# Optimization experiments

Measured on AMD Instinct MI355X. Metric: run time of the kernel, lower is better.

The kernel has to match this reference:

```python
import jax, jax.numpy as jnp
import numpy as np

B, T, V = 8, 1024, 2048

def setup_inputs() -> dict:
    key = jax.random.key(0)
    k1, k2, k3 = jax.random.split(key, 3)
    idx = jax.random.randint(k1, (B, T), 0, V)
    v_weight = jnp.zeros((T, 1), dtype=jnp.float32) + 0.02 * jax.random.normal(k2, (T, 1), dtype=jnp.float32)
    W = 0.01 * jnp.ones((V, V), dtype=jnp.float32) + 0.001 * jax.random.normal(k3, (V, V), dtype=jnp.float32)
    return {"idx": idx, "v_weight": v_weight, "W": W}

def reference(idx, v_weight, W):
    Tn = idx.shape[1]
    Vn = W.shape[0]
    e = jax.nn.one_hot(idx, Vn, dtype=jnp.float32)            # [B,T,V]
    pos = jnp.arange(Tn)
    rel = jnp.maximum(pos[:, None] - pos[None, :], 0)          # [T,T] clamped relative positions
    causal = pos[:, None] >= pos[None, :]                      # True where attention allowed
    # Layer 1: positional attention (shared across batch)
    a1 = v_weight[rel, 0]                                      # [T,T] gather from v embedding
    a1 = jnp.where(causal, a1, -jnp.inf)
    a1 = jax.nn.softmax(a1, axis=-1)
    layer_one = jnp.einsum('ts,bsv->btv', a1, e)               # [B,T,V]
    key_t = layer_one @ W.T                                    # Linear without bias: x @ W^T
    # Layer 2: content attention
    a2 = jnp.einsum('btv,bsv->bts', e, key_t)                  # [B,T,T]
    a2 = jnp.where(causal[None], a2, -jnp.inf)
    a2 = jax.nn.softmax(a2, axis=-1)
    logits = jnp.einsum('bts,bsv->btv', a2, e)                 # [B,T,V]
    return logits
```

## Files before the change

### kernel.cpp

```cpp
#include <hip/hip_runtime.h>
#include <hip/hip_bf16.h>
#include <math.h>

#define Bn 8
#define Tn 1024
#define Vn 2048

typedef __attribute__((ext_vector_type(8))) __bf16 bf16x8;
typedef __attribute__((ext_vector_type(4))) float floatx4;

__global__ __launch_bounds__(1024) void k_prep(const float* __restrict__ vw,
                                               float* __restrict__ E,
                                               float* __restrict__ Cinv) {
    __shared__ float sc[Tn];
    int tid = threadIdx.x;
    float e = __expf(vw[tid]);
    E[tid] = e;
    sc[tid] = e;
    __syncthreads();
    for (int off = 1; off < Tn; off <<= 1) {
        float add = (tid >= off) ? sc[tid - off] : 0.0f;
        __syncthreads();
        sc[tid] += add;
        __syncthreads();
    }
    Cinv[tid] = 1.0f / sc[tid];
}

__global__ __launch_bounds__(256) void k_bt(const float* __restrict__ E,
                                            const float* __restrict__ Cinv,
                                            __hip_bfloat16* __restrict__ BT) {
    int s = blockIdx.x;
    int tid = threadIdx.x;
    float cinv = Cinv[s];
    int k0 = tid * 4;
    ushort u[4];
#pragma unroll
    for (int j = 0; j < 4; ++j) {
        int k = k0 + j;
        float v = (k <= s) ? E[s - k] * cinv : 0.0f;
        __hip_bfloat16 h = __float2bfloat16(v);
        u[j] = *reinterpret_cast<ushort*>(&h);
    }
    *reinterpret_cast<ushort4*>(&BT[(size_t)s * Tn + k0]) = make_ushort4(u[0], u[1], u[2], u[3]);
}

__global__ __launch_bounds__(256) void k_gather(const int* __restrict__ idx,
                                                const float* __restrict__ W,
                                                __hip_bfloat16* __restrict__ A) {
    int b = blockIdx.y, t = blockIdx.x, tid = threadIdx.x;
    int r = idx[b * Tn + t];
    const float* Wr = W + (size_t)r * Vn;
    int4 c4 = *reinterpret_cast<const int4*>(&idx[b * Tn + tid * 4]);
    ushort u[4];
    __hip_bfloat16 h;
    h = __float2bfloat16(Wr[c4.x]); u[0] = *reinterpret_cast<ushort*>(&h);
    h = __float2bfloat16(Wr[c4.y]); u[1] = *reinterpret_cast<ushort*>(&h);
    h = __float2bfloat16(Wr[c4.z]); u[2] = *reinterpret_cast<ushort*>(&h);
    h = __float2bfloat16(Wr[c4.w]); u[3] = *reinterpret_cast<ushort*>(&h);
    *reinterpret_cast<ushort4*>(&A[((size_t)(b * Tn + t)) * Tn + tid * 4]) =
        make_ushort4(u[0], u[1], u[2], u[3]);
}

#define TM 128
#define TN 128
#define BK 32
#define LDP 40

__global__ __launch_bounds__(256) void k_gemm(const __hip_bfloat16* __restrict__ A,
                                              const __hip_bfloat16* __restrict__ BT,
                                              float* __restrict__ Cout) {
    __shared__ __align__(16) __hip_bfloat16 As[TM][LDP];
    __shared__ __align__(16) __hip_bfloat16 Bs[TN][LDP];
    int b = blockIdx.z;
    int m0 = blockIdx.y * TM;
    int n0 = blockIdx.x * TN;
    int tid = threadIdx.x;
    int wave = tid >> 6, lane = tid & 63;
    int wm = (wave >> 1) * 64, wn = (wave & 1) * 64;
    int lrow = lane & 15, quad = lane >> 4;

    const __hip_bfloat16* Ab = A + (size_t)b * Tn * Tn;

    floatx4 acc[4][4];
#pragma unroll
    for (int i = 0; i < 4; ++i)
#pragma unroll
        for (int j = 0; j < 4; ++j) acc[i][j] = (floatx4){0.f, 0.f, 0.f, 0.f};

    for (int k0 = 0; k0 < Tn; k0 += BK) {
#pragma unroll
        for (int i = 0; i < 2; ++i) {
            int ch = tid + i * 256;
            int r = ch >> 2, c = (ch & 3) * 8;
            *reinterpret_cast<uint4*>(&As[r][c]) =
                *reinterpret_cast<const uint4*>(&Ab[(size_t)(m0 + r) * Tn + k0 + c]);
            *reinterpret_cast<uint4*>(&Bs[r][c]) =
                *reinterpret_cast<const uint4*>(&BT[(size_t)(n0 + r) * Tn + k0 + c]);
        }
        __syncthreads();
        bf16x8 af[4], bfr[4];
#pragma unroll
        for (int mi = 0; mi < 4; ++mi)
            af[mi] = *reinterpret_cast<const bf16x8*>(&As[wm + mi * 16 + lrow][quad * 8]);
#pragma unroll
        for (int ni = 0; ni < 4; ++ni)
            bfr[ni] = *reinterpret_cast<const bf16x8*>(&Bs[wn + ni * 16 + lrow][quad * 8]);
#pragma unroll
        for (int mi = 0; mi < 4; ++mi)
#pragma unroll
            for (int ni = 0; ni < 4; ++ni)
                acc[mi][ni] = __builtin_amdgcn_mfma_f32_16x16x32_bf16(af[mi], bfr[ni],
                                                                      acc[mi][ni], 0, 0, 0);
        __syncthreads();
    }

    float* Cb = Cout + (size_t)b * Tn * Tn;
#pragma unroll
    for (int mi = 0; mi < 4; ++mi)
#pragma unroll
        for (int ni = 0; ni < 4; ++ni)
#pragma unroll
            for (int r = 0; r < 4; ++r) {
                int row = m0 + wm + mi * 16 + quad * 4 + r;
                int col = n0 + wn + ni * 16 + lrow;
                Cb[(size_t)row * Tn + col] = acc[mi][ni][r];
            }
}

__global__ __launch_bounds__(256) void k_softscat(const float* __restrict__ a2raw,
                                                  const int* __restrict__ idx,
                                                  float* __restrict__ out) {
    __shared__ float sh[Vn];
    __shared__ float red[8];
    int t = blockIdx.x, b = blockIdx.y, tid = threadIdx.x;
    int wave = tid >> 6, lane = tid & 63;
#pragma unroll
    for (int i = 0; i < Vn / 256; ++i) sh[tid + i * 256] = 0.0f;

    const float* row = a2raw + ((size_t)b * Tn + t) * Tn;
    float4 v4 = *reinterpret_cast<const float4*>(&row[tid * 4]);
    int4 c4 = *reinterpret_cast<const int4*>(&idx[b * Tn + tid * 4]);
    int s0 = tid * 4;
    float v[4] = {v4.x, v4.y, v4.z, v4.w};
    float m = -INFINITY;
#pragma unroll
    for (int j = 0; j < 4; ++j) {
        if (s0 + j > t) v[j] = -INFINITY;
        m = fmaxf(m, v[j]);
    }
#pragma unroll
    for (int off = 32; off > 0; off >>= 1) m = fmaxf(m, __shfl_xor(m, off));
    if (lane == 0) red[wave] = m;
    __syncthreads();
    m = fmaxf(fmaxf(red[0], red[1]), fmaxf(red[2], red[3]));
    float e[4];
    float lsum = 0.f;
#pragma unroll
    for (int j = 0; j < 4; ++j) {
        e[j] = (s0 + j <= t) ? __expf(v[j] - m) : 0.0f;
        lsum += e[j];
    }
#pragma unroll
    for (int off = 32; off > 0; off >>= 1) lsum += __shfl_xor(lsum, off);
    if (lane == 0) red[4 + wave] = lsum;
    __syncthreads();
    float inv = 1.0f / (red[4] + red[5] + red[6] + red[7]);
    int c[4] = {c4.x, c4.y, c4.z, c4.w};
#pragma unroll
    for (int j = 0; j < 4; ++j)
        if (s0 + j <= t) atomicAdd(&sh[c[j]], e[j] * inv);
    __syncthreads();
    float* orow = out + ((size_t)b * Tn + t) * Vn;
#pragma unroll
    for (int i = 0; i < Vn / (256 * 4); ++i)
        *reinterpret_cast<float4*>(&orow[(tid + i * 256) * 4]) =
            *reinterpret_cast<const float4*>(&sh[(tid + i * 256) * 4]);
}

extern "C" void kernel_launch(void* const* d_in, const int* in_sizes, int n_in,
                              void* d_out, int out_size, void* d_ws, size_t ws_size,
                              hipStream_t stream) {
    const int* idx = (const int*)d_in[0];
    const float* vw = (const float*)d_in[1];
    const float* W = (const float*)d_in[2];
    float* out = (float*)d_out;
    char* ws = (char*)d_ws;

    float* E = (float*)(ws);
    float* Cinv = (float*)(ws + 4096);
    __hip_bfloat16* BT = (__hip_bfloat16*)(ws + 8192);
    __hip_bfloat16* Abf = (__hip_bfloat16*)(ws + 2105344);
    float* a2raw = (float*)(ws + 18882560);

    k_prep<<<1, 1024, 0, stream>>>(vw, E, Cinv);
    k_bt<<<dim3(Tn), 256, 0, stream>>>(E, Cinv, BT);
    k_gather<<<dim3(Tn, Bn), 256, 0, stream>>>(idx, W, Abf);
    k_gemm<<<dim3(Tn / TN, Tn / TM, Bn), 256, 0, stream>>>(Abf, BT, a2raw);
    k_softscat<<<dim3(Tn, Bn), 256, 0, stream>>>(a2raw, idx, out);
}
```

Measured before the change: 159.6 us.

## Exploit causal structure: skip masked GEMM tiles, fuse prep into k_bt

The GEMM grid now covers only the 36 lower-triangular 128x128 tiles per batch, and each tile's K loop stops at the diagonal, because BT is zero above it. This removes roughly half the tiles plus the wasted K work. The separate single-block prefix-sum prep kernel is dropped: each k_bt block recomputes its own normalizer with a block reduction over exp(vw), and the softmax kernel skips loading masked-out score chunks. Upper-triangle entries of a2raw are left unwritten, which is safe because they are always masked before use.

Result: faster. 149.7 us (-6.2%).

```diff
diff --git a/kernel.cpp b/kernel.cpp
--- a/kernel.cpp
+++ b/kernel.cpp
@@ -9,36 +9,30 @@
 typedef __attribute__((ext_vector_type(8))) __bf16 bf16x8;
 typedef __attribute__((ext_vector_type(4))) float floatx4;
 
-__global__ __launch_bounds__(1024) void k_prep(const float* __restrict__ vw,
-                                               float* __restrict__ E,
-                                               float* __restrict__ Cinv) {
-    __shared__ float sc[Tn];
-    int tid = threadIdx.x;
-    float e = __expf(vw[tid]);
-    E[tid] = e;
-    sc[tid] = e;
-    __syncthreads();
-    for (int off = 1; off < Tn; off <<= 1) {
-        float add = (tid >= off) ? sc[tid - off] : 0.0f;
-        __syncthreads();
-        sc[tid] += add;
-        __syncthreads();
-    }
-    Cinv[tid] = 1.0f / sc[tid];
-}
-
-__global__ __launch_bounds__(256) void k_bt(const float* __restrict__ E,
-                                            const float* __restrict__ Cinv,
+__global__ __launch_bounds__(256) void k_bt(const float* __restrict__ vw,
                                             __hip_bfloat16* __restrict__ BT) {
+    __shared__ float red[4];
     int s = blockIdx.x;
     int tid = threadIdx.x;
-    float cinv = Cinv[s];
+    int wave = tid >> 6, lane = tid & 63;
+    float part = 0.0f;
+#pragma unroll
+    for (int i = 0; i < 4; ++i) {
+        int d = tid + i * 256;
+        if (d <= s) part += __expf(vw[d]);
+    }
+#pragma unroll
+    for (int off = 32; off > 0; off >>= 1) part += __shfl_xor(part, off);
+    if (lane == 0) red[wave] = part;
+    __syncthreads();
+    float cinv = 1.0f / (red[0] + red[1] + red[2] + red[3]);
+
     int k0 = tid * 4;
     ushort u[4];
 #pragma unroll
     for (int j = 0; j < 4; ++j) {
         int k = k0 + j;
-        float v = (k <= s) ? E[s - k] * cinv : 0.0f;
+        float v = (k <= s) ? __expf(vw[s - k]) * cinv : 0.0f;
         __hip_bfloat16 h = __float2bfloat16(v);
         u[j] = *reinterpret_cast<ushort*>(&h);
     }
@@ -66,15 +60,24 @@
 #define TN 128
 #define BK 32
 #define LDP 40
+#define NTILES 36
+
+__device__ const int TILE_MI[NTILES] = {7, 6,7, 5,6,7, 4,5,6,7, 3,4,5,6,7,
+                                        2,3,4,5,6,7, 1,2,3,4,5,6,7, 0,1,2,3,4,5,6,7};
+__device__ const int TILE_NI[NTILES] = {7, 6,6, 5,5,5, 4,4,4,4, 3,3,3,3,3,
+                                        2,2,2,2,2,2, 1,1,1,1,1,1,1, 0,0,0,0,0,0,0,0};
 
 __global__ __launch_bounds__(256) void k_gemm(const __hip_bfloat16* __restrict__ A,
                                               const __hip_bfloat16* __restrict__ BT,
                                               float* __restrict__ Cout) {
     __shared__ __align__(16) __hip_bfloat16 As[TM][LDP];
     __shared__ __align__(16) __hip_bfloat16 Bs[TN][LDP];
-    int b = blockIdx.z;
-    int m0 = blockIdx.y * TM;
-    int n0 = blockIdx.x * TN;
+    int b = blockIdx.x;
+    int tl = blockIdx.y;
+    int mi = TILE_MI[tl], ni = TILE_NI[tl];
+    int m0 = mi * TM;
+    int n0 = ni * TN;
+    int Kmax = (ni + 1) * TN;
     int tid = threadIdx.x;
     int wave = tid >> 6, lane = tid & 63;
     int wm = (wave >> 1) * 64, wn = (wave & 1) * 64;
@@ -88,7 +91,7 @@
 #pragma unroll
         for (int j = 0; j < 4; ++j) acc[i][j] = (floatx4){0.f, 0.f, 0.f, 0.f};
 
-    for (int k0 = 0; k0 < Tn; k0 += BK) {
+    for (int k0 = 0; k0 < Kmax; k0 += BK) {
 #pragma unroll
         for (int i = 0; i < 2; ++i) {
             int ch = tid + i * 256;
@@ -101,30 +104,30 @@
         __syncthreads();
         bf16x8 af[4], bfr[4];
 #pragma unroll
-        for (int mi = 0; mi < 4; ++mi)
-            af[mi] = *reinterpret_cast<const bf16x8*>(&As[wm + mi * 16 + lrow][quad * 8]);
-#pragma unroll
-        for (int ni = 0; ni < 4; ++ni)
-            bfr[ni] = *reinterpret_cast<const bf16x8*>(&Bs[wn + ni * 16 + lrow][quad * 8]);
-#pragma unroll
-        for (int mi = 0; mi < 4; ++mi)
-#pragma unroll
-            for (int ni = 0; ni < 4; ++ni)
-                acc[mi][ni] = __builtin_amdgcn_mfma_f32_16x16x32_bf16(af[mi], bfr[ni],
-                                                                      acc[mi][ni], 0, 0, 0);
+        for (int mi2 = 0; mi2 < 4; ++mi2)
+            af[mi2] = *reinterpret_cast<const bf16x8*>(&As[wm + mi2 * 16 + lrow][quad * 8]);
+#pragma unroll
+        for (int ni2 = 0; ni2 < 4; ++ni2)
+            bfr[ni2] = *reinterpret_cast<const bf16x8*>(&Bs[wn + ni2 * 16 + lrow][quad * 8]);
+#pragma unroll
+        for (int mi2 = 0; mi2 < 4; ++mi2)
+#pragma unroll
+            for (int ni2 = 0; ni2 < 4; ++ni2)
+                acc[mi2][ni2] = __builtin_amdgcn_mfma_f32_16x16x32_bf16(af[mi2], bfr[ni2],
+                                                                        acc[mi2][ni2], 0, 0, 0);
         __syncthreads();
     }
 
     float* Cb = Cout + (size_t)b * Tn * Tn;
 #pragma unroll
-    for (int mi = 0; mi < 4; ++mi)
-#pragma unroll
-        for (int ni = 0; ni < 4; ++ni)
+    for (int mi2 = 0; mi2 < 4; ++mi2)
+#pragma unroll
+        for (int ni2 = 0; ni2 < 4; ++ni2)
 #pragma unroll
             for (int r = 0; r < 4; ++r) {
-                int row = m0 + wm + mi * 16 + quad * 4 + r;
-                int col = n0 + wn + ni * 16 + lrow;
-                Cb[(size_t)row * Tn + col] = acc[mi][ni][r];
+                int row = m0 + wm + mi2 * 16 + quad * 4 + r;
+                int col = n0 + wn + ni2 * 16 + lrow;
+                Cb[(size_t)row * Tn + col] = acc[mi2][ni2][r];
             }
 }
 
@@ -139,10 +142,13 @@
     for (int i = 0; i < Vn / 256; ++i) sh[tid + i * 256] = 0.0f;
 
     const float* row = a2raw + ((size_t)b * Tn + t) * Tn;
-    float4 v4 = *reinterpret_cast<const float4*>(&row[tid * 4]);
-    int4 c4 = *reinterpret_cast<const int4*>(&idx[b * Tn + tid * 4]);
     int s0 = tid * 4;
-    float v[4] = {v4.x, v4.y, v4.z, v4.w};
+    float v[4] = {-INFINITY, -INFINITY, -INFINITY, -INFINITY};
+    if (s0 <= t) {
+        float4 v4 = *reinterpret_cast<const float4*>(&row[s0]);
+        v[0] = v4.x; v[1] = v4.y; v[2] = v4.z; v[3] = v4.w;
+    }
+    int4 c4 = *reinterpret_cast<const int4*>(&idx[b * Tn + s0]);
     float m = -INFINITY;
 #pragma unroll
     for (int j = 0; j < 4; ++j) {
@@ -187,15 +193,12 @@
     float* out = (float*)d_out;
     char* ws = (char*)d_ws;
 
-    float* E = (float*)(ws);
-    float* Cinv = (float*)(ws + 4096);
-    __hip_bfloat16* BT = (__hip_bfloat16*)(ws + 8192);
-    __hip_bfloat16* Abf = (__hip_bfloat16*)(ws + 2105344);
-    float* a2raw = (float*)(ws + 18882560);
-
-    k_prep<<<1, 1024, 0, stream>>>(vw, E, Cinv);
-    k_bt<<<dim3(Tn), 256, 0, stream>>>(E, Cinv, BT);
+    __hip_bfloat16* BT = (__hip_bfloat16*)(ws);
+    __hip_bfloat16* Abf = (__hip_bfloat16*)(ws + (2u << 20));
+    float* a2raw = (float*)(ws + (18u << 20));
+
+    k_bt<<<dim3(Tn), 256, 0, stream>>>(vw, BT);
     k_gather<<<dim3(Tn, Bn), 256, 0, stream>>>(idx, W, Abf);
-    k_gemm<<<dim3(Tn / TN, Tn / TM, Bn), 256, 0, stream>>>(Abf, BT, a2raw);
+    k_gemm<<<dim3(Bn, NTILES), 256, 0, stream>>>(Abf, BT, a2raw);
     k_softscat<<<dim3(Tn, Bn), 256, 0, stream>>>(a2raw, idx, out);
 }
```
